# Kernel tuning notes

Measured on AMD Instinct MI355X. Metric: run time of the kernel, lower is better.

## Reference

```python
import jax, jax.numpy as jnp
import numpy as np

B = 2_097_152  # batch of (ttm, logm) option quotes
J = 5          # hidden width from hidden_sizes=[5,5,5]


def setup_inputs() -> dict:
    key = jax.random.key(0)
    ks = jax.random.split(key, 14)
    d = jnp.float32
    s = 0.01  # torch init: normal(mean=0, std=0.01)
    inp = {
        "ttm": jax.random.uniform(ks[0], (B, 1), d),
        "logm": jax.random.normal(ks[1], (B, 1), d),
        "weights_logm": jax.random.normal(ks[2], (1, J), d) * s,
        "bias_logm": jax.random.normal(ks[3], (1, J), d) * s,
        "weights_ttm": jax.random.normal(ks[4], (1, J), d) * s,
        "bias_ttm": jax.random.normal(ks[5], (1, J), d) * s,
        "weights_exp": jax.random.normal(ks[6], (J, 1), d) * s,
        "bias_exp": jax.random.normal(ks[7], (1, J), d) * s,
        # nn.Linear default init ~ U(-1/sqrt(J), 1/sqrt(J))
        "W1": jax.random.uniform(ks[8], (J, J), d, -1.0, 1.0) / np.sqrt(J),
        "b1": jax.random.uniform(ks[9], (J,), d, -1.0, 1.0) / np.sqrt(J),
        "W2": jax.random.uniform(ks[10], (J, J), d, -1.0, 1.0) / np.sqrt(J),
        "b2": jax.random.uniform(ks[11], (J,), d, -1.0, 1.0) / np.sqrt(J),
        "Wo": jax.random.uniform(ks[12], (1, J), d, -1.0, 1.0) / np.sqrt(J),
        "bo": jax.random.uniform(ks[13], (1,), d, -1.0, 1.0) / np.sqrt(J),
    }
    return inp


def _forward(ttm, logm, weights_logm, bias_logm, weights_ttm, bias_ttm,
             weights_exp, bias_exp, W1, b1, W2, b2, Wo, bo):
    # smile transform of log-moneyness: sqrt(x*tanh(x+0.5) + tanh(-x/2) + 5e-4)
    x = bias_logm + logm @ jnp.exp(weights_logm)                     # [B, J]
    term_logm = jnp.sqrt(x * jnp.tanh(x + 0.5) + jnp.tanh(-x / 2) + 0.0005)
    term_ttm = jax.nn.sigmoid(bias_ttm + ttm @ jnp.exp(weights_ttm))  # [B, J]
    h = (term_logm * term_ttm) @ jnp.exp(weights_exp) + bias_exp      # [B,1]+[1,J] -> [B, J]
    h = jax.nn.softplus(h @ W1.T + b1)
    h = jax.nn.softplus(h @ W2.T + b2)
    return h @ Wo.T + bo                                              # [B, 1]


def reference(ttm, logm, weights_logm, bias_logm, weights_ttm, bias_ttm,
              weights_exp, bias_exp, W1, b1, W2, b2, Wo, bo):
    params = (weights_logm, bias_logm, weights_ttm, bias_ttm,
              weights_exp, bias_exp, W1, b1, W2, b2, Wo, bo)

    def out_sum(t, l):
        return jnp.sum(_forward(t, l, *params))

    output = _forward(ttm, logm, *params)                 # [B, 1]
    # grad of sum(output) wrt ttm and logm (rows independent -> per-sample grads)
    grad_ttm1, grad_logm1 = jax.grad(out_sum, argnums=(0, 1))(ttm, logm)
    # second derivative wrt logm: grad of sum(grad_logm1)
    grad_logm2 = jax.grad(
        lambda l: jnp.sum(jax.grad(out_sum, argnums=1)(ttm, l))
    )(logm)
    return (output, grad_ttm1, grad_logm1, grad_logm2)
```

## Files before the change

### kernel.cpp

```cpp
#include <hip/hip_runtime.h>
#include <math.h>

#define J 5

#if defined(__HIP_DEVICE_COMPILE__) && __has_builtin(__builtin_amdgcn_rcpf)
__device__ __forceinline__ float fastrcp(float x) { return __builtin_amdgcn_rcpf(x); }
#else
__device__ __forceinline__ float fastrcp(float x) { return 1.0f / x; }
#endif

#if defined(__HIP_DEVICE_COMPILE__) && __has_builtin(__builtin_amdgcn_rsqf)
__device__ __forceinline__ float fastrsq(float x) { return __builtin_amdgcn_rsqf(x); }
#else
__device__ __forceinline__ float fastrsq(float x) { return 1.0f / sqrtf(x); }
#endif

__global__ void setup_kernel(const float* __restrict__ w_logm, const float* __restrict__ b_logm,
                             const float* __restrict__ w_ttm,  const float* __restrict__ b_ttm,
                             const float* __restrict__ w_exp,  const float* __restrict__ b_exp,
                             const float* __restrict__ W1,     const float* __restrict__ b1,
                             const float* __restrict__ W2,     const float* __restrict__ b2,
                             const float* __restrict__ Wo,     const float* __restrict__ bo,
                             float* __restrict__ c)
{
    const int j = threadIdx.x;
    if (j >= J) return;
    const float ewl = __expf(w_logm[j]);
    const float ewt = __expf(w_ttm[j]);
    const float ewe = __expf(w_exp[j]);
    c[0  + j] = ewl;
    c[5  + j] = b_logm[j];
    c[10 + j] = ewl * ewl;
    c[15 + j] = -ewt;
    c[20 + j] = -b_ttm[j];
    c[25 + j] = ewe;
    c[30 + j] = ewt * ewe;
    float r = 0.0f, cc = b1[j];
#pragma unroll
    for (int t = 0; t < J; ++t) {
        const float w = W1[j * J + t];
        r += w;
        cc = fmaf(w, b_exp[t], cc);
    }
    c[35 + j] = r;
    c[40 + j] = cc;
    c[45 + j] = r * r;
#pragma unroll
    for (int t = 0; t < J; ++t) c[50 + j * J + t] = W2[j * J + t];
    c[75 + j] = b2[j];
    c[80 + j] = Wo[j];
    if (j == 0) c[85] = bo[0];
}

__device__ __forceinline__ void softplus_sig(float a, float& sp, float& sg) {
    const float aa = fabsf(a);
    const float em = __expf(-aa);
    const float w  = fastrcp(1.0f + em);
    sp = fmaxf(a, 0.0f) + __logf(1.0f + em);
    sg = (a >= 0.0f) ? w : 1.0f - w;
}

__global__ __launch_bounds__(256) void smile_main(
    const float* __restrict__ ttm, const float* __restrict__ logm,
    const float* __restrict__ c, float* __restrict__ out, int n)
{
    const int tid = blockIdx.x * blockDim.x + threadIdx.x;
    if (tid * 4 >= n) return;

    float ewl[J], bl[J], ewl2[J], newt[J], nbt[J], ewe[J], wte[J];
#pragma unroll
    for (int j = 0; j < J; ++j) {
        ewl[j]  = c[0  + j];
        bl[j]   = c[5  + j];
        ewl2[j] = c[10 + j];
        newt[j] = c[15 + j];
        nbt[j]  = c[20 + j];
        ewe[j]  = c[25 + j];
        wte[j]  = c[30 + j];
    }

    const float4 T4 = ((const float4*)ttm)[tid];
    const float4 L4 = ((const float4*)logm)[tid];
    const float Ts[4] = {T4.x, T4.y, T4.z, T4.w};
    const float Ls[4] = {L4.x, L4.y, L4.z, L4.w};

    float sA[4], sLA[4], sLLA[4], sTA[4];
#pragma unroll
    for (int k = 0; k < 4; ++k) {
        const float L = Ls[k], T = Ts[k];
        float s = 0.0f, sL = 0.0f, sLL = 0.0f, sT = 0.0f;
#pragma unroll
        for (int j = 0; j < J; ++j) {
            float x = fmaf(L, ewl[j], bl[j]);
            x = fminf(fmaxf(x, -30.0f), 30.0f);
            const float ex = __expf(x);
            const float e2 = ex * ex;
            const float t1 = fmaf(-2.0f, fastrcp(fmaf(2.7182818284590452f, e2, 1.0f)), 1.0f);
            const float t2 = (1.0f - ex) * fastrcp(1.0f + ex);
            const float m1 = fmaf(-t1, t1, 1.0f);
            const float m2 = fmaf(-t2, t2, 1.0f);
            const float u  = fmaf(x, t1, t2 + 5.0e-4f);
            const float xm1 = x * m1;
            const float ux  = fmaf(-0.5f, m2, t1 + xm1);
            const float uxx = fmaf(-0.5f * t2, m2, 2.0f * fmaf(-t1, xm1, m1));
            const float r   = fastrsq(u);
            const float tl  = u * r;
            const float i2  = 0.5f * r;
            const float h   = ux * (r * r);
            const float zn  = fmaf(T, newt[j], nbt[j]);
            const float tt  = fastrcp(1.0f + __expf(zn));
            const float dtt = fmaf(-tt, tt, tt);
            const float AA   = tt * ewe[j];
            const float ewlA = ewl[j] * AA;
            s   = fmaf(tl, AA, s);
            sL  = fmaf(ux * i2, ewlA, sL);
            const float inner = fmaf(-0.5f * ux, h, uxx);
            sLL = fmaf(inner * i2, ewl[j] * ewlA, sLL);
            sT  = fmaf(tl * dtt, wte[j], sT);
            (void)ewl2;
        }
        sA[k] = s; sLA[k] = sL; sLLA[k] = sLL; sTA[k] = sT;
    }

    float r1[J], c1[J], r1sq[J], W2r[J * J], b2[J], wo[J];
#pragma unroll
    for (int j = 0; j < J; ++j) {
        r1[j]   = c[35 + j];
        c1[j]   = c[40 + j];
        r1sq[j] = c[45 + j];
        b2[j]   = c[75 + j];
        wo[j]   = c[80 + j];
    }
#pragma unroll
    for (int t = 0; t < J * J; ++t) W2r[t] = c[50 + t];
    const float bo0 = c[85];

    float O0[4], O1[4], O2[4], O3[4];
#pragma unroll
    for (int k = 0; k < 4; ++k) {
        const float s = sA[k], sL = sLA[k], sLL = sLLA[k], sT = sTA[k];

        float q[J], p[J], sp1[J];
#pragma unroll
        for (int i = 0; i < J; ++i) {
            const float a = fmaf(s, r1[i], c1[i]);
            float sp, sg;
            softplus_sig(a, sp, sg);
            sp1[i] = sp;
            q[i]   = sg * r1[i];
            const float dsg = fmaf(-sg, sg, sg);
            p[i]   = dsg * r1sq[i];
        }

        float o = bo0, u1 = 0.0f, u2 = 0.0f, u3 = 0.0f;
#pragma unroll
        for (int i = 0; i < J; ++i) {
            float g = b2[i], Bq = 0.0f, Bp = 0.0f;
#pragma unroll
            for (int j = 0; j < J; ++j) {
                const float w = W2r[i * J + j];
                g  = fmaf(w, sp1[j], g);
                Bq = fmaf(w, q[j],   Bq);
                Bp = fmaf(w, p[j],   Bp);
            }
            float sp, sg;
            softplus_sig(g, sp, sg);
            const float dsg = fmaf(-sg, sg, sg);
            const float t   = wo[i] * sg;
            o  = fmaf(wo[i], sp, o);
            u1 = fmaf(t, Bq, u1);
            u2 = fmaf(t, Bp, u2);
            u3 = fmaf(wo[i] * dsg, Bq * Bq, u3);
        }
        O0[k] = o;
        O1[k] = sT * u1;
        O2[k] = sL * u1;
        O3[k] = fmaf(sL * sL, u3 + u2, sLL * u1);
    }

    ((float4*)(out))[tid]                 = make_float4(O0[0], O0[1], O0[2], O0[3]);
    ((float4*)(out + (size_t)n))[tid]     = make_float4(O1[0], O1[1], O1[2], O1[3]);
    ((float4*)(out + 2 * (size_t)n))[tid] = make_float4(O2[0], O2[1], O2[2], O2[3]);
    ((float4*)(out + 3 * (size_t)n))[tid] = make_float4(O3[0], O3[1], O3[2], O3[3]);
}

extern "C" void kernel_launch(void* const* d_in, const int* in_sizes, int n_in,
                              void* d_out, int out_size, void* d_ws, size_t ws_size,
                              hipStream_t stream) {
    const float* ttm    = (const float*)d_in[0];
    const float* logm   = (const float*)d_in[1];
    const float* w_logm = (const float*)d_in[2];
    const float* b_logm = (const float*)d_in[3];
    const float* w_ttm  = (const float*)d_in[4];
    const float* b_ttm  = (const float*)d_in[5];
    const float* w_exp  = (const float*)d_in[6];
    const float* b_exp  = (const float*)d_in[7];
    const float* W1     = (const float*)d_in[8];
    const float* b1     = (const float*)d_in[9];
    const float* W2     = (const float*)d_in[10];
    const float* b2     = (const float*)d_in[11];
    const float* Wo     = (const float*)d_in[12];
    const float* bo     = (const float*)d_in[13];
    float* out = (float*)d_out;
    float* cns = (float*)d_ws;

    const int n = in_sizes[0];
    setup_kernel<<<1, 64, 0, stream>>>(w_logm, b_logm, w_ttm, b_ttm, w_exp, b_exp,
                                       W1, b1, W2, b2, Wo, bo, cns);
    const int threads = (n + 3) / 4;
    const int blocks  = (threads + 255) / 256;
    smile_main<<<blocks, 256, 0, stream>>>(ttm, logm, cns, out, n);
}
```

Before: 135.0 us.

## Use base-2 exp/log intrinsics with prescaled constants and one element per thread

Prescales the constants by log2(e) in the setup kernel so the main kernel can call the hardware exp2/log2 intrinsics directly. It drops the clamp and the branchy stable softplus in favour of the unguarded log2(1+2^a) form. It also changes from four elements per thread with float4 loads and stores to one element per thread with scalar accesses, and sets an occupancy hint of 6 blocks in launch_bounds. The aim is fewer transcendental and ALU ops per element and higher occupancy, at the risk of overflow for large activations and less work per thread to amortise the uniform constant loads.

```diff
diff --git a/kernel.cpp b/kernel.cpp
--- a/kernel.cpp
+++ b/kernel.cpp
@@ -2,6 +2,8 @@
 #include <math.h>
 
 #define J 5
+#define LOG2E 1.4426950408889634f
+#define LN2   0.6931471805599453f
 
 #if defined(__HIP_DEVICE_COMPILE__) && __has_builtin(__builtin_amdgcn_rcpf)
 __device__ __forceinline__ float fastrcp(float x) { return __builtin_amdgcn_rcpf(x); }
@@ -13,6 +15,18 @@
 __device__ __forceinline__ float fastrsq(float x) { return __builtin_amdgcn_rsqf(x); }
 #else
 __device__ __forceinline__ float fastrsq(float x) { return 1.0f / sqrtf(x); }
+#endif
+
+#if defined(__HIP_DEVICE_COMPILE__) && __has_builtin(__builtin_amdgcn_exp2f)
+__device__ __forceinline__ float fexp2(float x) { return __builtin_amdgcn_exp2f(x); }
+#else
+__device__ __forceinline__ float fexp2(float x) { return exp2f(x); }
+#endif
+
+#if defined(__HIP_DEVICE_COMPILE__) && __has_builtin(__builtin_amdgcn_logf)
+__device__ __forceinline__ float flog2(float x) { return __builtin_amdgcn_logf(x); }
+#else
+__device__ __forceinline__ float flog2(float x) { return log2f(x); }
 #endif
 
 __global__ void setup_kernel(const float* __restrict__ w_logm, const float* __restrict__ b_logm,
@@ -28,11 +42,11 @@
     const float ewl = __expf(w_logm[j]);
     const float ewt = __expf(w_ttm[j]);
     const float ewe = __expf(w_exp[j]);
-    c[0  + j] = ewl;
-    c[5  + j] = b_logm[j];
-    c[10 + j] = ewl * ewl;
-    c[15 + j] = -ewt;
-    c[20 + j] = -b_ttm[j];
+    c[0  + j] = ewl * LOG2E;
+    c[5  + j] = b_logm[j] * LOG2E;
+    c[10 + j] = ewl;
+    c[15 + j] = -ewt * LOG2E;
+    c[20 + j] = -b_ttm[j] * LOG2E;
     c[25 + j] = ewe;
     c[30 + j] = ewt * ewe;
     float r = 0.0f, cc = b1[j];
@@ -43,145 +57,129 @@
         cc = fmaf(w, b_exp[t], cc);
     }
     c[35 + j] = r;
-    c[40 + j] = cc;
-    c[45 + j] = r * r;
-#pragma unroll
-    for (int t = 0; t < J; ++t) c[50 + j * J + t] = W2[j * J + t];
-    c[75 + j] = b2[j];
-    c[80 + j] = Wo[j];
-    if (j == 0) c[85] = bo[0];
+    c[40 + j] = r * LOG2E;
+    c[45 + j] = cc * LOG2E;
+    c[50 + j] = r * r;
+#pragma unroll
+    for (int t = 0; t < J; ++t) c[55 + j * J + t] = W2[j * J + t];
+    c[80 + j] = b2[j] * LOG2E;
+    c[85 + j] = Wo[j];
+    c[90 + j] = Wo[j] * LN2;
+    if (j == 0) c[95] = bo[0];
 }
 
-__device__ __forceinline__ void softplus_sig(float a, float& sp, float& sg) {
-    const float aa = fabsf(a);
-    const float em = __expf(-aa);
-    const float w  = fastrcp(1.0f + em);
-    sp = fmaxf(a, 0.0f) + __logf(1.0f + em);
-    sg = (a >= 0.0f) ? w : 1.0f - w;
-}
-
-__global__ __launch_bounds__(256) void smile_main(
+__global__ __launch_bounds__(256, 6) void smile_main(
     const float* __restrict__ ttm, const float* __restrict__ logm,
     const float* __restrict__ c, float* __restrict__ out, int n)
 {
     const int tid = blockIdx.x * blockDim.x + threadIdx.x;
-    if (tid * 4 >= n) return;
-
-    float ewl[J], bl[J], ewl2[J], newt[J], nbt[J], ewe[J], wte[J];
+    if (tid >= n) return;
+
+    const float T = ttm[tid];
+    const float L = logm[tid];
+
+    float ewlb[J], blb[J], ewl[J], newtb[J], nbtb[J], ewe[J], wte[J];
 #pragma unroll
     for (int j = 0; j < J; ++j) {
-        ewl[j]  = c[0  + j];
-        bl[j]   = c[5  + j];
-        ewl2[j] = c[10 + j];
-        newt[j] = c[15 + j];
-        nbt[j]  = c[20 + j];
-        ewe[j]  = c[25 + j];
-        wte[j]  = c[30 + j];
-    }
-
-    const float4 T4 = ((const float4*)ttm)[tid];
-    const float4 L4 = ((const float4*)logm)[tid];
-    const float Ts[4] = {T4.x, T4.y, T4.z, T4.w};
-    const float Ls[4] = {L4.x, L4.y, L4.z, L4.w};
-
-    float sA[4], sLA[4], sLLA[4], sTA[4];
-#pragma unroll
-    for (int k = 0; k < 4; ++k) {
-        const float L = Ls[k], T = Ts[k];
-        float s = 0.0f, sL = 0.0f, sLL = 0.0f, sT = 0.0f;
-#pragma unroll
-        for (int j = 0; j < J; ++j) {
-            float x = fmaf(L, ewl[j], bl[j]);
-            x = fminf(fmaxf(x, -30.0f), 30.0f);
-            const float ex = __expf(x);
-            const float e2 = ex * ex;
-            const float t1 = fmaf(-2.0f, fastrcp(fmaf(2.7182818284590452f, e2, 1.0f)), 1.0f);
-            const float t2 = (1.0f - ex) * fastrcp(1.0f + ex);
-            const float m1 = fmaf(-t1, t1, 1.0f);
-            const float m2 = fmaf(-t2, t2, 1.0f);
-            const float u  = fmaf(x, t1, t2 + 5.0e-4f);
-            const float xm1 = x * m1;
-            const float ux  = fmaf(-0.5f, m2, t1 + xm1);
-            const float uxx = fmaf(-0.5f * t2, m2, 2.0f * fmaf(-t1, xm1, m1));
-            const float r   = fastrsq(u);
-            const float tl  = u * r;
-            const float i2  = 0.5f * r;
-            const float h   = ux * (r * r);
-            const float zn  = fmaf(T, newt[j], nbt[j]);
-            const float tt  = fastrcp(1.0f + __expf(zn));
-            const float dtt = fmaf(-tt, tt, tt);
-            const float AA   = tt * ewe[j];
-            const float ewlA = ewl[j] * AA;
-            s   = fmaf(tl, AA, s);
-            sL  = fmaf(ux * i2, ewlA, sL);
-            const float inner = fmaf(-0.5f * ux, h, uxx);
-            sLL = fmaf(inner * i2, ewl[j] * ewlA, sLL);
-            sT  = fmaf(tl * dtt, wte[j], sT);
-            (void)ewl2;
-        }
-        sA[k] = s; sLA[k] = sL; sLLA[k] = sLL; sTA[k] = sT;
-    }
-
-    float r1[J], c1[J], r1sq[J], W2r[J * J], b2[J], wo[J];
+        ewlb[j]  = c[0  + j];
+        blb[j]   = c[5  + j];
+        ewl[j]   = c[10 + j];
+        newtb[j] = c[15 + j];
+        nbtb[j]  = c[20 + j];
+        ewe[j]   = c[25 + j];
+        wte[j]   = c[30 + j];
+    }
+
+    float s = 0.0f, sL = 0.0f, sLL = 0.0f, sT = 0.0f;
+#pragma unroll
+    for (int j = 0; j < J; ++j) {
+        const float x2 = fmaf(L, ewlb[j], blb[j]);
+        const float ex = fexp2(x2);
+        const float x  = x2 * LN2;
+        const float e2 = ex * ex;
+        const float w1 = fastrcp(fmaf(2.7182818284590452f, e2, 1.0f));
+        const float t1 = fmaf(-2.0f, w1, 1.0f);
+        const float w2 = fastrcp(1.0f + ex);
+        const float t2 = fmaf(2.0f, w2, -1.0f);
+        const float m1 = fmaf(-t1, t1, 1.0f);
+        const float m2 = fmaf(-t2, t2, 1.0f);
+        const float u  = fmaf(x, t1, t2 + 5.0e-4f);
+        const float xm1 = x * m1;
+        const float ux  = fmaf(-0.5f, m2, t1 + xm1);
+        const float f1  = fmaf(-t1, xm1, m1);
+        const float uxx = fmaf(-0.5f * t2, m2, f1 + f1);
+        const float r   = fastrsq(u);
+        const float tl  = u * r;
+        const float i2  = 0.5f * r;
+        const float h   = ux * (r * r);
+        const float tt  = fastrcp(1.0f + fexp2(fmaf(T, newtb[j], nbtb[j])));
+        const float dtt = fmaf(-tt, tt, tt);
+        const float AA   = tt * ewe[j];
+        const float ewlA = ewl[j] * AA;
+        s  = fmaf(tl, AA, s);
+        const float G = ux * i2;
+        sL = fmaf(G, ewlA, sL);
+        const float inner = fmaf(-0.5f * ux, h, uxx);
+        sLL = fmaf(inner * i2, ewl[j] * ewlA, sLL);
+        sT  = fmaf(tl * dtt, wte[j], sT);
+    }
+
+    float r1[J], r1b[J], c1b[J], r1sq[J], W2r[J * J], b2b[J], wo[J], wob[J];
 #pragma unroll
     for (int j = 0; j < J; ++j) {
         r1[j]   = c[35 + j];
-        c1[j]   = c[40 + j];
-        r1sq[j] = c[45 + j];
-        b2[j]   = c[75 + j];
-        wo[j]   = c[80 + j];
-    }
-#pragma unroll
-    for (int t = 0; t < J * J; ++t) W2r[t] = c[50 + t];
-    const float bo0 = c[85];
-
-    float O0[4], O1[4], O2[4], O3[4];
-#pragma unroll
-    for (int k = 0; k < 4; ++k) {
-        const float s = sA[k], sL = sLA[k], sLL = sLLA[k], sT = sTA[k];
-
-        float q[J], p[J], sp1[J];
-#pragma unroll
-        for (int i = 0; i < J; ++i) {
-            const float a = fmaf(s, r1[i], c1[i]);
-            float sp, sg;
-            softplus_sig(a, sp, sg);
-            sp1[i] = sp;
-            q[i]   = sg * r1[i];
-            const float dsg = fmaf(-sg, sg, sg);
-            p[i]   = dsg * r1sq[i];
+        r1b[j]  = c[40 + j];
+        c1b[j]  = c[45 + j];
+        r1sq[j] = c[50 + j];
+        b2b[j]  = c[80 + j];
+        wo[j]   = c[85 + j];
+        wob[j]  = c[90 + j];
+    }
+#pragma unroll
+    for (int t = 0; t < J * J; ++t) W2r[t] = c[55 + t];
+    const float bo0 = c[95];
+
+    float sp2[J], q[J], p[J];
+#pragma unroll
+    for (int i = 0; i < J; ++i) {
+        const float a2 = fmaf(s, r1b[i], c1b[i]);
+        const float ex = fexp2(a2);
+        const float d  = 1.0f + ex;
+        const float w  = fastrcp(d);
+        const float sg = 1.0f - w;
+        sp2[i] = flog2(d);
+        q[i]   = sg * r1[i];
+        p[i]   = (w * sg) * r1sq[i];
+    }
+
+    float o = bo0, u1 = 0.0f, u2 = 0.0f, u3 = 0.0f;
+#pragma unroll
+    for (int i = 0; i < J; ++i) {
+        float g2 = b2b[i], Bq = 0.0f, Bp = 0.0f;
+#pragma unroll
+        for (int j = 0; j < J; ++j) {
+            const float w = W2r[i * J + j];
+            g2 = fmaf(w, sp2[j], g2);
+            Bq = fmaf(w, q[j],   Bq);
+            Bp = fmaf(w, p[j],   Bp);
         }
-
-        float o = bo0, u1 = 0.0f, u2 = 0.0f, u3 = 0.0f;
-#pragma unroll
-        for (int i = 0; i < J; ++i) {
-            float g = b2[i], Bq = 0.0f, Bp = 0.0f;
-#pragma unroll
-            for (int j = 0; j < J; ++j) {
-                const float w = W2r[i * J + j];
-                g  = fmaf(w, sp1[j], g);
-                Bq = fmaf(w, q[j],   Bq);
-                Bp = fmaf(w, p[j],   Bp);
-            }
-            float sp, sg;
-            softplus_sig(g, sp, sg);
-            const float dsg = fmaf(-sg, sg, sg);
-            const float t   = wo[i] * sg;
-            o  = fmaf(wo[i], sp, o);
-            u1 = fmaf(t, Bq, u1);
-            u2 = fmaf(t, Bp, u2);
-            u3 = fmaf(wo[i] * dsg, Bq * Bq, u3);
-        }
-        O0[k] = o;
-        O1[k] = sT * u1;
-        O2[k] = sL * u1;
-        O3[k] = fmaf(sL * sL, u3 + u2, sLL * u1);
-    }
-
-    ((float4*)(out))[tid]                 = make_float4(O0[0], O0[1], O0[2], O0[3]);
-    ((float4*)(out + (size_t)n))[tid]     = make_float4(O1[0], O1[1], O1[2], O1[3]);
-    ((float4*)(out + 2 * (size_t)n))[tid] = make_float4(O2[0], O2[1], O2[2], O2[3]);
-    ((float4*)(out + 3 * (size_t)n))[tid] = make_float4(O3[0], O3[1], O3[2], O3[3]);
+        const float ex = fexp2(g2);
+        const float d  = 1.0f + ex;
+        const float w  = fastrcp(d);
+        const float sg = 1.0f - w;
+        const float dsg = w * sg;
+        o  = fmaf(wob[i], flog2(d), o);
+        const float t = wo[i] * sg;
+        u1 = fmaf(t, Bq, u1);
+        u2 = fmaf(t, Bp, u2);
+        u3 = fmaf(wo[i] * dsg, Bq * Bq, u3);
+    }
+
+    const size_t nn = (size_t)n;
+    out[tid]          = o;
+    out[nn + tid]     = sT * u1;
+    out[2 * nn + tid] = sL * u1;
+    out[3 * nn + tid] = fmaf(sL * sL, u3 + u2, sLL * u1);
 }
 
 extern "C" void kernel_launch(void* const* d_in, const int* in_sizes, int n_in,
@@ -207,7 +205,6 @@
     const int n = in_sizes[0];
     setup_kernel<<<1, 64, 0, stream>>>(w_logm, b_logm, w_ttm, b_ttm, w_exp, b_exp,
                                        W1, b1, W2, b2, Wo, bo, cns);
-    const int threads = (n + 3) / 4;
-    const int blocks  = (threads + 255) / 256;
+    const int blocks = (n + 255) / 256;
     smile_main<<<blocks, 256, 0, stream>>>(ttm, logm, cns, out, n);
 }
```

Measured after the change: 121.7 us. 9.9% less time.
